# Optimization experiments

Hardware: AMD Instinct MI355X
Metric: run time of the kernel (lower is better)

The kernel has to match this reference:

```python
import jax, jax.numpy as jnp
import numpy as np

N_SAMPLES = 2 ** 15          # 32768
STEP = 256                   # transform_step_size
WIN = 2048                   # transform/synthesis window
N_FRAMES = N_SAMPLES // STEP # 128
N_COEFFS = WIN // 2 + 1      # 1025
DILATIONS = (1, 2, 4, 8, 16, 32, 64, 1)


def hann(n):
    return 0.5 - 0.5 * jnp.cos(2.0 * jnp.pi * jnp.arange(n, dtype=jnp.float32) / n)


def transform(audio):
    # audio: (B, 1, N) -> magnitude STFT (B, 1024, 128)
    x = audio[:, 0, :]
    x = jnp.pad(x, ((0, 0), (0, WIN - STEP)))  # pad so n_frames == N_SAMPLES // STEP
    idx = np.arange(N_FRAMES)[:, None] * STEP + np.arange(WIN)[None, :]
    frames = x[:, idx] * hann(WIN)
    spec = jnp.abs(jnp.fft.rfft(frames, norm='ortho'))   # (B, F, 1025)
    return spec[..., : N_COEFFS - 1].transpose(0, 2, 1)  # (B, 1024, F)


def conv1x1(x, w, b):
    # x: (B, I, T), w: (O, I, 1), b: (O,)
    return jnp.einsum('oi,bit->bot', w[:, :, 0], x) + b[None, :, None]


def anticausal_block(x, w, b, dilation):
    # kernel_size=2 anti-causal dilated conv: looks at t and t+dilation (pad future)
    x_fut = jnp.pad(x, ((0, 0), (0, 0), (0, dilation)))[:, :, dilation:]
    y = (jnp.einsum('oi,bit->bot', w[:, :, 0], x)
         + jnp.einsum('oi,bit->bot', w[:, :, 1], x_fut)
         + b[None, :, None])
    y = jax.nn.leaky_relu(y, 0.2)
    y = y + x
    # do_norm: per-example max-norm
    y = y / (jnp.max(jnp.abs(y), axis=(1, 2), keepdims=True) + 1e-8)
    return y


def upsample_with_holes(x, desired_size):
    # zero-stuffing upsample: out[..., ::step] = x
    b, c, t = x.shape
    step = desired_size // t
    out = jnp.zeros((b, c, desired_size), x.dtype)
    return out.at[:, :, ::step].set(x)


def freq_domain_resonance(coeffs):
    # coeffs: (1, C, 1025) in [0, 1); per-frame decay = repeated spectral multiply
    c = jnp.clip(coeffs, 0.0, 0.9999)
    exps = jnp.arange(1, N_FRAMES + 1, dtype=coeffs.dtype)
    mags = c[:, :, None, :] ** exps[None, None, :, None]     # (1, C, F, 1025)
    frames = jnp.fft.irfft(mags, n=WIN) * hann(WIN)
    hop = WIN // 2
    total = hop * (N_FRAMES - 1) + WIN
    idx = np.arange(N_FRAMES)[:, None] * hop + np.arange(WIN)[None, :]
    out = jnp.zeros(frames.shape[:2] + (total,), frames.dtype)
    out = out.at[:, :, idx].add(frames)                      # overlap-add
    return out[..., :N_SAMPLES]                              # (1, C, N)


def fft_convolve(a, b):
    # circular-free conv via zero-padding to 2N, keep first N (matches repo fft_convolve)
    n = a.shape[-1]
    spec = jnp.fft.rfft(a, n=2 * n) * jnp.fft.rfft(b, n=2 * n)
    return jnp.fft.irfft(spec, n=2 * n)[..., :n]


def reference(audio, proj_in_w, proj_in_b, blocks_w, blocks_b,
              proj_sparse_w, proj_sparse_b, proj_dense_w, proj_dense_b, resonances):
    spec = transform(audio)                         # (B, 1024, 128)
    h = conv1x1(spec, proj_in_w, proj_in_b)         # (B, 32, 128)
    acc = jnp.zeros_like(h)
    for i, d in enumerate(DILATIONS):               # fixed 8-block stack
        h = anticausal_block(h, blocks_w[i], blocks_b[i], d)
        acc = acc + h
    x = conv1x1(acc, proj_sparse_w, proj_sparse_b)  # (B, 256, 128)
    sparse = jax.nn.relu(x)
    x = conv1x1(sparse, proj_dense_w, proj_dense_b) # (B, 32, 128)
    x = upsample_with_holes(x, N_SAMPLES)           # (B, 32, 32768)
    res = freq_domain_resonance(resonances)         # (1, 32, 32768), broadcast over B
    y = fft_convolve(x, res)                        # (B, 32, 32768)
    y = jnp.sum(y, axis=1, keepdims=True)           # (B, 1, 32768)
    return y, sparse


def setup_inputs() -> dict:
    key = jax.random.key(0)
    ks = jax.random.split(key, 12)
    u = lambda k, shape: jax.random.uniform(k, shape, jnp.float32, -0.05, 0.05)
    return {
        'audio': jax.random.normal(ks[0], (32, 1, N_SAMPLES), jnp.float32),
        'proj_in_w': u(ks[1], (32, 1024, 1)),
        'proj_in_b': jnp.zeros((32,), jnp.float32),
        'blocks_w': u(ks[2], (8, 32, 32, 2)),
        'blocks_b': jnp.zeros((8, 32), jnp.float32),
        'proj_sparse_w': u(ks[3], (256, 32, 1)),
        'proj_sparse_b': jnp.zeros((256,), jnp.float32),
        'proj_dense_w': u(ks[4], (32, 256, 1)),
        'proj_dense_b': jnp.zeros((32,), jnp.float32),
        'resonances': jax.random.uniform(ks[5], (1, 32, N_COEFFS), jnp.float32, 0.0, 1.0),
    }
```

## Files before the change

kernel.cpp:

```cpp
#include <hip/hip_runtime.h>

#define PI_F 3.14159265358979323846f

typedef short bf16x8 __attribute__((ext_vector_type(8)));
typedef float f32x4 __attribute__((ext_vector_type(4)));

#define MFMA16(acc, a, b) \
  acc = __builtin_amdgcn_mfma_f32_16x16x32_bf16(a, b, acc, 0, 0, 0)

#define WS_SPEC   0u
#define WS_H0     4194304u
#define WS_ACC    4325376u
#define WS_V      4456448u
#define WS_WTIN   4587520u
#define WS_WST    4620288u
#define WS_WDT    4628480u
#define WS_FRAMES 4636672u
#define WS_RES    6733824u

#define BFLY(I0, I1, C, S)                                   \
  { float2 u = buf[I0]; float2 w = buf[I1];                  \
    float tr = (C) * w.x - (S) * w.y;                        \
    float ti = (C) * w.y + (S) * w.x;                        \
    buf[I0] = make_float2(u.x + tr, u.y + ti);               \
    buf[I1] = make_float2(u.x - tr, u.y - ti); }

__device__ __forceinline__ void fft2048_stages(float2* buf, int tid) {
  for (int t = tid; t < 1024; t += 256) {
    int i0 = 2 * t, i1 = i0 + 1;
    float2 u = buf[i0], w = buf[i1];
    buf[i0] = make_float2(u.x + w.x, u.y + w.y);
    buf[i1] = make_float2(u.x - w.x, u.y - w.y);
  }
  __syncthreads();
  for (int t = tid; t < 1024; t += 256) {
    int j  = t & 1;
    int i0 = ((t >> 1) << 2) + j, i1 = i0 + 2;
    float2 u = buf[i0], w = buf[i1];
    float tr = j ? w.y : w.x;
    float ti = j ? -w.x : w.y;
    buf[i0] = make_float2(u.x + tr, u.y + ti);
    buf[i1] = make_float2(u.x - tr, u.y - ti);
  }
  __syncthreads();
  for (int t = tid; t < 1024; t += 256) {
    int j  = t & 3;
    int i0 = ((t >> 2) << 3) + j, i1 = i0 + 4;
    const float R = 0.7071067811865476f;
    float c = (j == 0) ? 1.f : ((j == 1) ? R : ((j == 2) ? 0.f : -R));
    float s = (j == 0) ? 0.f : ((j == 2) ? -1.f : -R);
    BFLY(i0, i1, c, s);
  }
  __syncthreads();
  for (int stage = 3; stage <= 8; ++stage) {
    int half = 1 << stage;
    int j = tid & (half - 1);
    float s, c;
    __sincosf(-PI_F / (float)half * (float)j, &s, &c);
    for (int t = tid; t < 1024; t += 256) {
      int i0 = ((t >> stage) << (stage + 1)) + j;
      int i1 = i0 + half;
      BFLY(i0, i1, c, s);
    }
    __syncthreads();
  }
  {
    float s, c;
    __sincosf(-PI_F / 512.f * (float)tid, &s, &c);
    BFLY(tid,        tid + 512,  c, s);
    BFLY(1024 + tid, 1536 + tid, c, s);
    BFLY(tid + 256,  tid + 768,  s, -c);
    BFLY(1280 + tid, 1792 + tid, s, -c);
  }
  __syncthreads();
  {
    float s0, c0;
    __sincosf(-PI_F / 1024.f * (float)tid, &s0, &c0);
    const float R = 0.7071067811865476f;
    BFLY(tid,       tid + 1024, c0, s0);
    BFLY(tid + 256, tid + 1280, R * (c0 + s0), R * (s0 - c0));
    BFLY(tid + 512, tid + 1536, s0, -c0);
    BFLY(tid + 768, tid + 1792, R * (s0 - c0), -R * (s0 + c0));
  }
  __syncthreads();
}

__global__ __launch_bounds__(256) void k_fft(const float* __restrict__ audio,
                                             const float* __restrict__ resin,
                                             const float* __restrict__ Win,
                                             const float* __restrict__ Ws,
                                             const float* __restrict__ Wd,
                                             const float* __restrict__ bwIn,
                                             float* __restrict__ spec,
                                             float* __restrict__ frames,
                                             float* __restrict__ WT,
                                             float* __restrict__ WsT,
                                             float* __restrict__ WdT,
                                             short* __restrict__ Whg,
                                             short* __restrict__ Wlg) {
  __shared__ float2 buf[2048];
  int blk = blockIdx.x;

  if (blk >= 2560) {
    int i = (blk - 2560) * 256 + threadIdx.x;
    if (i < 32768) { int o = i >> 10, k = i & 1023; WT[k * 32 + o] = Win[i]; }
    if (i < 8192)  { int o2 = i >> 5, m = i & 31;   WsT[m * 256 + o2] = Ws[i]; }
    if (i < 8192)  { int c = i >> 8, o2 = i & 255;  WdT[o2 * 32 + c] = Wd[i]; }
    if (i < 16384) {
      int w = i & 1, m = (i >> 1) & 31, o = (i >> 6) & 31, s = i >> 11;
      float val = bwIn[i];
      unsigned bits = __float_as_uint(val);
      float rem = val - __uint_as_float(bits & 0xffff0000u);
      int row = (s * 2 + w) * 32 + o;
      Whg[row * 32 + m] = (short)(bits >> 16);
      Wlg[row * 32 + m] = (short)(__float_as_uint(rem) >> 16);
    }
    return;
  }

  if (blk < 2048) {
    int b  = blk >> 6;
    int f0 = (blk & 63) * 2;
    for (int j = threadIdx.x; j < 2048; j += 256) {
      float h = 0.5f - 0.5f * __cosf(0.0030679615757712823f * (float)j);
      int i1 = f0 * 256 + j;
      int i2 = i1 + 256;
      float a1 = (i1 < 32768) ? audio[b * 32768 + i1] : 0.f;
      float a2 = (i2 < 32768) ? audio[b * 32768 + i2] : 0.f;
      buf[__brev((unsigned)j) >> 21] = make_float2(a1 * h, a2 * h);
    }
    __syncthreads();
    fft2048_stages(buf, threadIdx.x);
    const float scale = 0.5f * 0.022097086912079608f;
    for (int k = threadIdx.x; k < 1024; k += 256) {
      float2 zk = buf[k];
      float2 zn = buf[(2048 - k) & 2047];
      float f1r = zk.x + zn.x, f1i = zk.y - zn.y;
      float f2r = zk.y + zn.y, f2i = zk.x - zn.x;
      spec[(b * 128 + f0) * 1024 + k]     = sqrtf(f1r * f1r + f1i * f1i) * scale;
      spec[(b * 128 + f0 + 1) * 1024 + k] = sqrtf(f2r * f2r + f2i * f2i) * scale;
    }
  } else {
    int r = blk - 2048;
    int c = r >> 4;
    int g = r & 15;
    float e1 = (float)(2 * g + 1);
    for (int k = threadIdx.x; k < 2048; k += 256) {
      int kk = (k <= 1024) ? k : 2048 - k;
      float cv = resin[c * 1025 + kk];
      cv = fminf(fmaxf(cv, 0.f), 0.9999f);
      float m1 = __powf(cv, e1);
      float m2 = m1 * cv;
      buf[__brev((unsigned)k) >> 21] = make_float2(m1, m2);
    }
    __syncthreads();
    fft2048_stages(buf, threadIdx.x);
    for (int j = threadIdx.x; j < 2048; j += 256) {
      float h  = 0.5f - 0.5f * __cosf(0.0030679615757712823f * (float)j);
      float sc = h * (1.f / 2048.f);
      float2 z = buf[j];
      frames[(c * 32 + 2 * g) * 2048 + j]     = z.x * sc;
      frames[(c * 32 + 2 * g + 1) * 2048 + j] = z.y * sc;
    }
  }
}

__global__ __launch_bounds__(256) void k_proj_in(const float* __restrict__ spec,
                                                 const float* __restrict__ WT,
                                                 const float* __restrict__ bias,
                                                 float* __restrict__ h0) {
  __shared__ float specL[8][1024];
  __shared__ float red[32][8][8];
  int b  = blockIdx.x >> 4;
  int t0 = (blockIdx.x & 15) * 8;
  for (int i = threadIdx.x; i < 8192; i += 256) {
    int tt = i >> 10, k = i & 1023;
    specL[tt][k] = spec[(b * 128 + t0 + tt) * 1024 + k];
  }
  __syncthreads();
  int o = threadIdx.x & 31, p = threadIdx.x >> 5;
  float part[8] = {0.f,0.f,0.f,0.f,0.f,0.f,0.f,0.f};
  for (int i = 0; i < 128; ++i) {
    int k = p * 128 + ((i + p * 4) & 127);
    float w = WT[k * 32 + o];
#pragma unroll
    for (int tt = 0; tt < 8; ++tt) part[tt] += w * specL[tt][k];
  }
#pragma unroll
  for (int tt = 0; tt < 8; ++tt) red[o][tt][p] = part[tt];
  __syncthreads();
  int oo = threadIdx.x >> 3, tt2 = threadIdx.x & 7;
  float s = bias[oo];
#pragma unroll
  for (int p2 = 0; p2 < 8; ++p2) s += red[oo][tt2][p2];
  h0[b * 4096 + oo * 128 + t0 + tt2] = s;
}

__global__ __launch_bounds__(256) void k_obpack(const float* __restrict__ frames,
                                                short* __restrict__ Bh,
                                                short* __restrict__ Bl) {
  int c = blockIdx.x >> 4, o = blockIdx.x & 15;
  int r = threadIdx.x;
  bf16x8 hv, lv;
#pragma unroll
  for (int j = 0; j < 8; ++j) {
    int fo = 8 * o + j;
    int g  = fo >> 2;
    int j0 = ((fo & 3) << 8) + r;
    float val = frames[(c * 32 + g) * 2048 + j0];
    if (g > 0) val += frames[(c * 32 + g - 1) * 2048 + j0 + 1024];
    unsigned bits = __float_as_uint(val);
    float rem = val - __uint_as_float(bits & 0xffff0000u);
    hv[j] = (short)(bits >> 16);
    lv[j] = (short)(__float_as_uint(rem) >> 16);
  }
  int unit = (blockIdx.x * 16 + (r >> 4)) * 16 + (r & 15);
  ((bf16x8*)Bh)[unit] = hv;
  ((bf16x8*)Bl)[unit] = lv;
}

__global__ __launch_bounds__(1024) void k_chain(const float* __restrict__ h0,
                                                const short* __restrict__ Whg,
                                                const short* __restrict__ Wlg,
                                                const float* __restrict__ bb,
                                                float* __restrict__ accout) {
  __shared__ __align__(16) short Hh[192 * 40];
  __shared__ __align__(16) short Hl[192 * 40];
  __shared__ float Hf[128 * 33];
  __shared__ float bL[256];
  __shared__ float red[16];
  int b = blockIdx.x, tid = threadIdx.x;

  for (int i = tid; i < 4096; i += 1024) {
    int t = i & 127;
    int o = i >> 7;
    float val = h0[b * 4096 + i];
    Hf[t * 33 + o] = val;
    unsigned bits = __float_as_uint(val);
    float rem = val - __uint_as_float(bits & 0xffff0000u);
    Hh[t * 40 + o] = (short)(bits >> 16);
    Hl[t * 40 + o] = (short)(__float_as_uint(rem) >> 16);
  }
  for (int i = tid; i < 64 * 40; i += 1024) {
    Hh[128 * 40 + i] = 0;
    Hl[128 * 40 + i] = 0;
  }
  if (tid < 256) bL[tid] = bb[tid];
  __syncthreads();

  int wave = tid >> 6, lane = tid & 63;
  int quad = lane >> 4, l15 = lane & 15;
  int t0 = (wave & 7) * 16, o0 = (wave >> 3) * 16;
  int tD = t0 + quad * 4;
  int oD = o0 + l15;

  const bf16x8* Hh8 = (const bf16x8*)Hh;
  const bf16x8* Hl8 = (const bf16x8*)Hl;
  const bf16x8* Wh8 = (const bf16x8*)Whg;
  const bf16x8* Wl8 = (const bf16x8*)Wlg;

  float accsum[4] = {0.f, 0.f, 0.f, 0.f};
  const int DIL[8] = {1, 2, 4, 8, 16, 32, 64, 1};

#pragma unroll
  for (int s = 0; s < 8; ++s) {
    int arow = t0 + l15;
    int frow = arow + DIL[s];
    bf16x8 Ah = Hh8[arow * 5 + quad];
    bf16x8 Al = Hl8[arow * 5 + quad];
    bf16x8 Fh = Hh8[frow * 5 + quad];
    bf16x8 Fl = Hl8[frow * 5 + quad];
    int w0row = ((s * 2 + 0) * 32 + oD) * 4 + quad;
    int w1row = ((s * 2 + 1) * 32 + oD) * 4 + quad;
    bf16x8 B0h = Wh8[w0row], B0l = Wl8[w0row];
    bf16x8 B1h = Wh8[w1row], B1l = Wl8[w1row];
    float bias = bL[s * 32 + oD];
    f32x4 acc = {bias, bias, bias, bias};
    MFMA16(acc, Ah, B0h); MFMA16(acc, Ah, B0l); MFMA16(acc, Al, B0h);
    MFMA16(acc, Fh, B1h); MFMA16(acc, Fh, B1l); MFMA16(acc, Fl, B1h);
    float hnew[4], lmax = 0.f;
#pragma unroll
    for (int r = 0; r < 4; ++r) {
      float sv = acc[r];
      sv = (sv > 0.f) ? sv : 0.2f * sv;
      sv += Hf[(tD + r) * 33 + oD];
      hnew[r] = sv;
      lmax = fmaxf(lmax, fabsf(sv));
    }
#pragma unroll
    for (int off = 32; off > 0; off >>= 1)
      lmax = fmaxf(lmax, __shfl_down(lmax, off, 64));
    if (lane == 0) red[wave] = lmax;
    __syncthreads();
    float mx = red[0];
#pragma unroll
    for (int i = 1; i < 16; ++i) mx = fmaxf(mx, red[i]);
    float nm = 1.f / (mx + 1e-8f);
#pragma unroll
    for (int r = 0; r < 4; ++r) {
      float hv = hnew[r] * nm;
      accsum[r] += hv;
      int t = tD + r;
      Hf[t * 33 + oD] = hv;
      unsigned bits = __float_as_uint(hv);
      float rem = hv - __uint_as_float(bits & 0xffff0000u);
      Hh[t * 40 + oD] = (short)(bits >> 16);
      Hl[t * 40 + oD] = (short)(__float_as_uint(rem) >> 16);
    }
    __syncthreads();
  }
#pragma unroll
  for (int r = 0; r < 4; ++r)
    accout[b * 4096 + (tD + r) * 32 + oD] = accsum[r];
}

__global__ __launch_bounds__(256) void k_sparse_dense(const float* __restrict__ acc,
                                                      const float* __restrict__ WsT,
                                                      const float* __restrict__ bs,
                                                      const float* __restrict__ WdT,
                                                      const float* __restrict__ bd,
                                                      float* __restrict__ out_sparse,
                                                      float* __restrict__ v) {
  __shared__ float accL[4][32];
  __shared__ float sL[4][256];
  __shared__ float red[8][4][32];
  int b = blockIdx.x >> 5, tq = blockIdx.x & 31;
  int t0 = tq * 4;
  int tid = threadIdx.x;
  if (tid < 128)
    accL[tid >> 5][tid & 31] = acc[b * 4096 + (t0 + (tid >> 5)) * 32 + (tid & 31)];
  __syncthreads();
  float bsv = bs[tid];
  float s0 = bsv, s1 = bsv, s2 = bsv, s3 = bsv;
  for (int m = 0; m < 32; ++m) {
    float w = WsT[m * 256 + tid];
    s0 += w * accL[0][m]; s1 += w * accL[1][m];
    s2 += w * accL[2][m]; s3 += w * accL[3][m];
  }
  s0 = fmaxf(s0, 0.f); s1 = fmaxf(s1, 0.f); s2 = fmaxf(s2, 0.f); s3 = fmaxf(s3, 0.f);
  float* os = out_sparse + b * 32768 + tid * 128 + t0;
  os[0] = s0; os[1] = s1; os[2] = s2; os[3] = s3;
  sL[0][tid] = s0; sL[1][tid] = s1; sL[2][tid] = s2; sL[3][tid] = s3;
  __syncthreads();
  int c = tid & 31, p = tid >> 5;
  float p0 = 0.f, p1 = 0.f, p2 = 0.f, p3 = 0.f;
  for (int jj = 0; jj < 32; ++jj) {
    int o2 = p * 32 + jj;
    float w = WdT[o2 * 32 + c];
    p0 += w * sL[0][o2]; p1 += w * sL[1][o2];
    p2 += w * sL[2][o2]; p3 += w * sL[3][o2];
  }
  red[p][0][c] = p0; red[p][1][c] = p1; red[p][2][c] = p2; red[p][3][c] = p3;
  __syncthreads();
  if (tid < 128) {
    int tt = tid >> 5, cc = tid & 31;
    float vv = bd[cc];
#pragma unroll
    for (int p2i = 0; p2i < 8; ++p2i) vv += red[p2i][tt][cc];
    v[b * 4096 + cc * 128 + t0 + tt] = vv;
  }
}

__global__ __launch_bounds__(512, 4) void k_conv(const float* __restrict__ v,
                                                 const short* __restrict__ Bh,
                                                 const short* __restrict__ Bl,
                                                 float* __restrict__ y) {
  __shared__ __align__(16) short AH[32 * 264];
  __shared__ __align__(16) short AL[32 * 264];
  __shared__ float vwin[2][16][48];

  int xcd  = blockIdx.x & 7;
  int slot = blockIdx.x >> 3;
  int e, b;
  if      (slot < 32) { e = xcd;      b = slot; }
  else if (slot < 64) { e = xcd + 8;  b = slot - 32; }
  else                { e = (xcd < 4) ? (xcd + 16) : (xcd + 12);
                        b = (xcd < 4) ? (slot - 64) : (slot - 48); }
  int j, uc;
  if      (e < 2)  { j = 0; uc = e; }
  else if (e < 6)  { j = 1; uc = e - 2; }
  else if (e < 12) { j = 2; uc = e - 6; }
  else             { j = 3; uc = e - 12; }
  int D0 = 32 * j - 16 * uc;

  for (int i = threadIdx.x; i < 1504; i += 512) {
    int ii = i % 47;
    int r  = i / 47;
    int c  = r & 15, ph = r >> 4;
    int d  = D0 - 15 + ii;
    vwin[ph][c][ii] = (d >= 0 && d < 128)
        ? v[b * 4096 + (16 * ph + c) * 128 + d] : 0.f;
  }
  __syncthreads();

  int lane = threadIdx.x & 63, wave = threadIdx.x >> 6;
  int quad = lane >> 4, l15 = lane & 15;
  int cq   = quad >> 1;
  int og   = 2 * uc + (quad & 1);
  int nt0  = wave * 2;

  f32x4 acc00 = (f32x4)0.f, acc01 = (f32x4)0.f;
  f32x4 acc10 = (f32x4)0.f, acc11 = (f32x4)0.f;

  const bf16x8* AH8 = (const bf16x8*)AH;
  const bf16x8* AL8 = (const bf16x8*)AL;
  const bf16x8* Bh8 = (const bf16x8*)Bh;
  const bf16x8* Bl8 = (const bf16x8*)Bl;
  short2* AH2 = (short2*)AH;
  short2* AL2 = (short2*)AL;

  int abase0 = (0 * 16 + l15) * 33 + quad;
  int abase1 = (1 * 16 + l15) * 33 + quad;

  for (int p = 0; p < 2; ++p) {
    for (int i = threadIdx.x; i < 4096; i += 512) {
      int kk2 = i & 127;
      int row = i >> 7;
      int cl  = kk2 >> 3;
      int uu  = (kk2 & 7) * 2;
      int ii  = row - uu + 15;
      float v0 = vwin[p][cl][ii];
      float v1 = vwin[p][cl][ii - 1];
      unsigned w0 = __float_as_uint(v0), w1 = __float_as_uint(v1);
      float r0 = v0 - __uint_as_float(w0 & 0xffff0000u);
      float r1 = v1 - __uint_as_float(w1 & 0xffff0000u);
      int u2 = row * 132 + kk2;
      AH2[u2] = make_short2((short)(w0 >> 16), (short)(w1 >> 16));
      AL2[u2] = make_short2((short)(__float_as_uint(r0) >> 16),
                            (short)(__float_as_uint(r1) >> 16));
    }
    __syncthreads();

#pragma unroll
    for (int ks = 0; ks < 8; ++ks) {
      bf16x8 ah0 = AH8[abase0 + ks * 4];
      bf16x8 al0 = AL8[abase0 + ks * 4];
      bf16x8 ah1 = AH8[abase1 + ks * 4];
      bf16x8 al1 = AL8[abase1 + ks * 4];
      int c   = 16 * p + 2 * ks + cq;
      int bb0 = (c * 16 + og) * 256 + l15;
      bf16x8 bh0 = Bh8[bb0 + nt0 * 16];
      bf16x8 bl0 = Bl8[bb0 + nt0 * 16];
      bf16x8 bh1 = Bh8[bb0 + (nt0 + 1) * 16];
      bf16x8 bl1 = Bl8[bb0 + (nt0 + 1) * 16];
      MFMA16(acc00, ah0, bh0); MFMA16(acc00, ah0, bl0); MFMA16(acc00, al0, bh0);
      MFMA16(acc10, ah1, bh0); MFMA16(acc10, ah1, bl0); MFMA16(acc10, al1, bh0);
      MFMA16(acc01, ah0, bh1); MFMA16(acc01, ah0, bl1); MFMA16(acc01, al0, bh1);
      MFMA16(acc11, ah1, bh1); MFMA16(acc11, ah1, bl1); MFMA16(acc11, al1, bh1);
    }
    __syncthreads();
  }

  {
    float* yb0 = y + b * 32768 + (32 * j + 0 * 16 + quad * 4) * 256 + l15;
    float* yb1 = y + b * 32768 + (32 * j + 1 * 16 + quad * 4) * 256 + l15;
#pragma unroll
    for (int reg = 0; reg < 4; ++reg) {
      atomicAdd(yb0 + reg * 256 + (nt0 + 0) * 16, acc00[reg]);
      atomicAdd(yb0 + reg * 256 + (nt0 + 1) * 16, acc01[reg]);
      atomicAdd(yb1 + reg * 256 + (nt0 + 0) * 16, acc10[reg]);
      atomicAdd(yb1 + reg * 256 + (nt0 + 1) * 16, acc11[reg]);
    }
  }
}

extern "C" void kernel_launch(void* const* d_in, const int* in_sizes, int n_in,
                              void* d_out, int out_size, void* d_ws, size_t ws_size,
                              hipStream_t stream) {
  const float* audio = (const float*)d_in[0];
  const float* Win   = (const float*)d_in[1];
  const float* bin   = (const float*)d_in[2];
  const float* bw    = (const float*)d_in[3];
  const float* bb    = (const float*)d_in[4];
  const float* Ws    = (const float*)d_in[5];
  const float* bs    = (const float*)d_in[6];
  const float* Wd    = (const float*)d_in[7];
  const float* bd    = (const float*)d_in[8];
  const float* reson = (const float*)d_in[9];

  float* out = (float*)d_out;
  float* ws  = (float*)d_ws;

  float* spec   = ws + WS_SPEC;
  float* h0     = ws + WS_H0;
  float* accb   = ws + WS_ACC;
  float* vbuf   = ws + WS_V;
  float* WT     = ws + WS_WTIN;
  float* WsT    = ws + WS_WST;
  float* WdT    = ws + WS_WDT;
  float* frames = ws + WS_FRAMES;
  short* Bh = (short*)(ws + WS_RES);
  short* Bl = (short*)(ws + WS_RES + 524288u);
  short* Whg = (short*)(ws + WS_V);
  short* Wlg = (short*)(ws + WS_V + 8192u);

  hipMemsetAsync(d_out, 0, 1048576u * sizeof(float), stream);

  k_fft<<<2688, 256, 0, stream>>>(audio, reson, Win, Ws, Wd, bw,
                                  spec, frames, WT, WsT, WdT, Whg, Wlg);
  k_obpack<<<512, 256, 0, stream>>>(frames, Bh, Bl);
  k_proj_in<<<512, 256, 0, stream>>>(spec, WT, bin, h0);
  k_chain<<<32, 1024, 0, stream>>>(h0, Whg, Wlg, bb, accb);
  k_sparse_dense<<<1024, 256, 0, stream>>>(accb, WsT, bs, WdT, bd, out + 1048576, vbuf);
  k_conv<<<640, 512, 0, stream>>>(vbuf, Bh, Bl, out);
}
```

Measured before the change: 188.6 us.

## Use radix-4 FFT stages and padded shared-memory indexing in the FFT kernel

Replaces the radix-2 stages of the 2048-point shared-memory FFT with fused radix-4 passes. This roughly halves the number of LDS round trips and __syncthreads barriers per transform. It also pads the shared buffer with one extra slot every 16 entries to reduce bank conflicts on strided butterfly accesses. The cost is more registers per thread, a slightly larger LDS footprint, and extra index arithmetic.

```diff
diff --git a/kernel.cpp b/kernel.cpp
--- a/kernel.cpp
+++ b/kernel.cpp
@@ -18,6 +18,8 @@
 #define WS_FRAMES 4636672u
 #define WS_RES    6733824u
 
+#define BIX(a) ((a) + ((a) >> 4))
+
 #define BFLY(I0, I1, C, S)                                   \
   { float2 u = buf[I0]; float2 w = buf[I1];                  \
     float tr = (C) * w.x - (S) * w.y;                        \
@@ -25,62 +27,73 @@
     buf[I0] = make_float2(u.x + tr, u.y + ti);               \
     buf[I1] = make_float2(u.x - tr, u.y - ti); }
 
+__device__ __forceinline__ void quad_bfly(float2* buf, int a, int h,
+                                          float cs, float ss, float cp, float sp) {
+  float2 x0 = buf[BIX(a)],         x1 = buf[BIX(a + h)];
+  float2 x2 = buf[BIX(a + 2 * h)], x3 = buf[BIX(a + 3 * h)];
+  float t1x = cs * x1.x - ss * x1.y, t1y = cs * x1.y + ss * x1.x;
+  float t3x = cs * x3.x - ss * x3.y, t3y = cs * x3.y + ss * x3.x;
+  float2 y0 = make_float2(x0.x + t1x, x0.y + t1y);
+  float2 y1 = make_float2(x0.x - t1x, x0.y - t1y);
+  float2 y2 = make_float2(x2.x + t3x, x2.y + t3y);
+  float2 y3 = make_float2(x2.x - t3x, x2.y - t3y);
+  float u2x = cp * y2.x - sp * y2.y, u2y = cp * y2.y + sp * y2.x;
+  float u3x = sp * y3.x + cp * y3.y, u3y = sp * y3.y - cp * y3.x;
+  buf[BIX(a)]         = make_float2(y0.x + u2x, y0.y + u2y);
+  buf[BIX(a + 2 * h)] = make_float2(y0.x - u2x, y0.y - u2y);
+  buf[BIX(a + h)]     = make_float2(y1.x + u3x, y1.y + u3y);
+  buf[BIX(a + 3 * h)] = make_float2(y1.x - u3x, y1.y - u3y);
+}
+
 __device__ __forceinline__ void fft2048_stages(float2* buf, int tid) {
-  for (int t = tid; t < 1024; t += 256) {
-    int i0 = 2 * t, i1 = i0 + 1;
-    float2 u = buf[i0], w = buf[i1];
-    buf[i0] = make_float2(u.x + w.x, u.y + w.y);
-    buf[i1] = make_float2(u.x - w.x, u.y - w.y);
-  }
-  __syncthreads();
-  for (int t = tid; t < 1024; t += 256) {
-    int j  = t & 1;
-    int i0 = ((t >> 1) << 2) + j, i1 = i0 + 2;
-    float2 u = buf[i0], w = buf[i1];
-    float tr = j ? w.y : w.x;
-    float ti = j ? -w.x : w.y;
-    buf[i0] = make_float2(u.x + tr, u.y + ti);
-    buf[i1] = make_float2(u.x - tr, u.y - ti);
-  }
-  __syncthreads();
-  for (int t = tid; t < 1024; t += 256) {
-    int j  = t & 3;
-    int i0 = ((t >> 2) << 3) + j, i1 = i0 + 4;
-    const float R = 0.7071067811865476f;
-    float c = (j == 0) ? 1.f : ((j == 1) ? R : ((j == 2) ? 0.f : -R));
-    float s = (j == 0) ? 0.f : ((j == 2) ? -1.f : -R);
-    BFLY(i0, i1, c, s);
-  }
-  __syncthreads();
-  for (int stage = 3; stage <= 8; ++stage) {
-    int half = 1 << stage;
-    int j = tid & (half - 1);
-    float s, c;
-    __sincosf(-PI_F / (float)half * (float)j, &s, &c);
-    for (int t = tid; t < 1024; t += 256) {
-      int i0 = ((t >> stage) << (stage + 1)) + j;
-      int i1 = i0 + half;
-      BFLY(i0, i1, c, s);
-    }
-    __syncthreads();
-  }
+  const float R = 0.7071067811865476f;
+  for (int g = tid; g < 512; g += 256) {
+    int a = g << 2;
+    float2 x0 = buf[BIX(a)],     x1 = buf[BIX(a + 1)];
+    float2 x2 = buf[BIX(a + 2)], x3 = buf[BIX(a + 3)];
+    float2 y0 = make_float2(x0.x + x1.x, x0.y + x1.y);
+    float2 y1 = make_float2(x0.x - x1.x, x0.y - x1.y);
+    float2 y2 = make_float2(x2.x + x3.x, x2.y + x3.y);
+    float2 y3 = make_float2(x2.x - x3.x, x2.y - x3.y);
+    buf[BIX(a)]     = make_float2(y0.x + y2.x, y0.y + y2.y);
+    buf[BIX(a + 2)] = make_float2(y0.x - y2.x, y0.y - y2.y);
+    buf[BIX(a + 1)] = make_float2(y1.x + y3.y, y1.y - y3.x);
+    buf[BIX(a + 3)] = make_float2(y1.x - y3.y, y1.y + y3.x);
+  }
+  __syncthreads();
   {
-    float s, c;
-    __sincosf(-PI_F / 512.f * (float)tid, &s, &c);
-    BFLY(tid,        tid + 512,  c, s);
-    BFLY(1024 + tid, 1536 + tid, c, s);
-    BFLY(tid + 256,  tid + 768,  s, -c);
-    BFLY(1280 + tid, 1792 + tid, s, -c);
-  }
-  __syncthreads();
+    int j = tid & 3;
+    const float C8 = 0.9238795325112867f, S8 = 0.3826834323650898f;
+    float cs = (j == 0) ? 1.f : ((j == 1) ? R : ((j == 2) ? 0.f : -R));
+    float ss = (j == 0) ? 0.f : ((j == 2) ? -1.f : -R);
+    float cp = (j == 0) ? 1.f : ((j == 1) ? C8 : ((j == 2) ? R : S8));
+    float sp = (j == 0) ? 0.f : ((j == 1) ? -S8 : ((j == 2) ? -R : -C8));
+    for (int g = tid; g < 512; g += 256) {
+      int a = ((g >> 2) << 4) + j;
+      quad_bfly(buf, a, 4, cs, ss, cp, sp);
+    }
+  }
+  __syncthreads();
+#pragma unroll
+  for (int s = 4; s <= 8; s += 2) {
+    int h = 1 << s;
+    int j = tid & (h - 1);
+    float ss, cs, sp, cp;
+    __sincosf(-PI_F / (float)h * (float)j, &ss, &cs);
+    __sincosf(-PI_F / (float)(2 * h) * (float)j, &sp, &cp);
+    for (int g = tid; g < 512; g += 256) {
+      int a = ((g >> s) << (s + 2)) + j;
+      quad_bfly(buf, a, h, cs, ss, cp, sp);
+    }
+    __syncthreads();
+  }
   {
     float s0, c0;
     __sincosf(-PI_F / 1024.f * (float)tid, &s0, &c0);
-    const float R = 0.7071067811865476f;
-    BFLY(tid,       tid + 1024, c0, s0);
-    BFLY(tid + 256, tid + 1280, R * (c0 + s0), R * (s0 - c0));
-    BFLY(tid + 512, tid + 1536, s0, -c0);
-    BFLY(tid + 768, tid + 1792, R * (s0 - c0), -R * (s0 + c0));
+    BFLY(BIX(tid),       BIX(tid + 1024), c0, s0);
+    BFLY(BIX(tid + 256), BIX(tid + 1280), R * (c0 + s0), R * (s0 - c0));
+    BFLY(BIX(tid + 512), BIX(tid + 1536), s0, -c0);
+    BFLY(BIX(tid + 768), BIX(tid + 1792), R * (s0 - c0), -R * (s0 + c0));
   }
   __syncthreads();
 }
@@ -98,7 +111,7 @@
                                              float* __restrict__ WdT,
                                              short* __restrict__ Whg,
                                              short* __restrict__ Wlg) {
-  __shared__ float2 buf[2048];
+  __shared__ float2 buf[2176];
   int blk = blockIdx.x;
 
   if (blk >= 2560) {
@@ -127,14 +140,14 @@
       int i2 = i1 + 256;
       float a1 = (i1 < 32768) ? audio[b * 32768 + i1] : 0.f;
       float a2 = (i2 < 32768) ? audio[b * 32768 + i2] : 0.f;
-      buf[__brev((unsigned)j) >> 21] = make_float2(a1 * h, a2 * h);
+      buf[BIX(__brev((unsigned)j) >> 21)] = make_float2(a1 * h, a2 * h);
     }
     __syncthreads();
     fft2048_stages(buf, threadIdx.x);
     const float scale = 0.5f * 0.022097086912079608f;
     for (int k = threadIdx.x; k < 1024; k += 256) {
-      float2 zk = buf[k];
-      float2 zn = buf[(2048 - k) & 2047];
+      float2 zk = buf[BIX(k)];
+      float2 zn = buf[BIX((2048 - k) & 2047)];
       float f1r = zk.x + zn.x, f1i = zk.y - zn.y;
       float f2r = zk.y + zn.y, f2i = zk.x - zn.x;
       spec[(b * 128 + f0) * 1024 + k]     = sqrtf(f1r * f1r + f1i * f1i) * scale;
@@ -151,14 +164,14 @@
       cv = fminf(fmaxf(cv, 0.f), 0.9999f);
       float m1 = __powf(cv, e1);
       float m2 = m1 * cv;
-      buf[__brev((unsigned)k) >> 21] = make_float2(m1, m2);
+      buf[BIX(__brev((unsigned)k) >> 21)] = make_float2(m1, m2);
     }
     __syncthreads();
     fft2048_stages(buf, threadIdx.x);
     for (int j = threadIdx.x; j < 2048; j += 256) {
       float h  = 0.5f - 0.5f * __cosf(0.0030679615757712823f * (float)j);
       float sc = h * (1.f / 2048.f);
-      float2 z = buf[j];
+      float2 z = buf[BIX(j)];
       frames[(c * 32 + 2 * g) * 2048 + j]     = z.x * sc;
       frames[(c * 32 + 2 * g + 1) * 2048 + j] = z.y * sc;
     }
```

Measured after the change: 181.3 us. 3.9% less time.
